# Performance work log

Measured on AMD Instinct MI355X. Metric: run time of the kernel, lower is better.

Reference implementation:

```python
import jax, jax.numpy as jnp
import numpy as np

N = 4096        # atoms
F = 128         # node feature channels (MACE hidden irreps scalar channels)
K = 8           # radial basis size
NELEM = 10      # chemical elements
RMAX = 5.0      # cutoff (Angstrom), model.r_max
BOX = 34.5      # box side -> ~0.1 atoms/A^3, ~50 neighbors within RMAX


def setup_inputs() -> dict:
    key = jax.random.key(0)
    ks = jax.random.split(key, 7)
    positions = jax.random.uniform(ks[0], (N, 3), jnp.float32) * BOX
    z = jax.random.randint(ks[1], (N,), 0, NELEM)
    embed = jax.random.normal(ks[2], (NELEM, F), jnp.float32) * 0.1
    W1 = jax.random.normal(ks[3], (K, F, F), jnp.float32) / np.sqrt(K * F)
    W2 = jax.random.normal(ks[4], (K, F, F), jnp.float32) / np.sqrt(K * F)
    Wr1 = jax.random.normal(ks[5], (F, F), jnp.float32) / np.sqrt(F)
    Wr2 = jax.random.normal(ks[6], (F, 1), jnp.float32) / np.sqrt(F)
    return dict(positions=positions, z=z, embed=embed, W1=W1, W2=W2, Wr1=Wr1, Wr2=Wr2)


def _energy(positions, embed, W1, W2, Wr1, Wr2, z):
    # node embedding from atomic species (node_attrs one-hot @ embedding)
    h = embed[z]                                            # [N,F]
    # --- neighborlist: radius graph with self-edge masking (pbc = False) ---
    sq = jnp.sum(positions * positions, axis=-1)            # [N]
    d2 = sq[:, None] + sq[None, :] - 2.0 * (positions @ positions.T)  # [N,N]
    eye = jnp.eye(positions.shape[0], dtype=bool)
    d2_safe = jnp.where(eye | (d2 <= 0), 1.0, d2)           # avoid sqrt(0) grad
    d = jnp.sqrt(d2_safe)                                   # [N,N]
    mask = (d < RMAX) & (~eye) & (d2 > 0)                   # keep_edge = ~true_self_edge
    # smooth cutoff envelope
    env = jnp.where(mask, 0.5 * (jnp.cos(jnp.pi * d / RMAX) + 1.0), 0.0)  # [N,N]
    # Gaussian radial basis
    mus = jnp.linspace(0.0, RMAX, K, dtype=jnp.float32)     # [K]
    gamma = jnp.float32((K / RMAX) ** 2)
    rbf = jnp.exp(-gamma * (d[..., None] - mus) ** 2) * env[..., None]    # [N,N,K]
    # --- two message-passing layers (radial-weighted neighbor aggregation) ---
    for W in (W1, W2):
        A = jnp.einsum('ijk,jf->ikf', rbf, h)               # [N,K,F] gather-scatter agg
        h = jax.nn.silu(jnp.einsum('ikf,kfg->ig', A, W) + h)  # [N,F]
    # --- per-atom energy readout, summed over graph ---
    e_atom = (jax.nn.silu(h @ Wr1) @ Wr2)[:, 0]             # [N]
    return jnp.sum(e_atom)


def reference(positions, z, embed, W1, W2, Wr1, Wr2):
    energy, dE_dpos = jax.value_and_grad(_energy)(positions, embed, W1, W2, Wr1, Wr2, z)
    forces = -dE_dpos                                       # [N,3]
    return energy, forces
```

## Files before the change

kernel.cpp:

```cpp
#include <hip/hip_runtime.h>
#include <math.h>

#define N_ATOMS 4096
#define F 128
#define K 8
#define KF 1024
#define KFF 131072
#define FF 16384
#define NF 524288
#define NF4 131072
#define NKF 4194304
#define MAXNB 128
#define RMAX 5.0f
#define GAMMA 2.56f
#define MU_STEP 0.714285714285714f
#define PI_F 3.14159265358979323846f
#define POR (PI_F / RMAX)

typedef __bf16 bf16x8_t __attribute__((ext_vector_type(8)));
typedef float f32x4_t __attribute__((ext_vector_type(4)));
typedef unsigned short u16x8_t __attribute__((ext_vector_type(8)));
typedef unsigned short u16x4_t __attribute__((ext_vector_type(4)));

__device__ __forceinline__ float sigm(float x){ return 1.0f/(1.0f + expf(-x)); }
__device__ __forceinline__ unsigned short f2bf(float x){
  unsigned int u = __float_as_uint(x);
  u += 0x7fff + ((u >> 16) & 1);
  return (unsigned short)(u >> 16);
}

__global__ __launch_bounds__(256) void k_nb(const float* __restrict__ pos,
        int* __restrict__ nb_idx, float* __restrict__ nb_d, int* __restrict__ nb_cnt){
  int t = threadIdx.x;
  int w = t >> 6, lane = t & 63;
  int i = blockIdx.x*4 + w;
  __shared__ float spx[256], spy[256], spz[256], ssq[256];
  float pix = pos[3*i], piy = pos[3*i+1], piz = pos[3*i+2];
  float sqi = pix*pix + piy*piy + piz*piz;
  int count = 0;
  for (int jb = 0; jb < N_ATOMS; jb += 256){
    __syncthreads();
    float px = pos[3*(jb+t)], py = pos[3*(jb+t)+1], pz = pos[3*(jb+t)+2];
    spx[t] = px; spy[t] = py; spz[t] = pz;
    ssq[t] = px*px + py*py + pz*pz;
    __syncthreads();
    #pragma unroll
    for (int c = 0; c < 4; c++){
      int jj = c*64 + lane;
      int j = jb + jj;
      float dot = pix*spx[jj] + piy*spy[jj] + piz*spz[jj];
      float d2 = sqi + ssq[jj] - 2.0f*dot;
      float d = sqrtf(d2);
      bool pred = (j != i) && (d2 > 0.0f) && (d < RMAX);
      unsigned long long m = __ballot(pred);
      int off = __popcll(m & ((1ull << lane) - 1ull));
      if (pred){
        int p = count + off;
        if (p < MAXNB){ nb_idx[i*MAXNB + p] = j; nb_d[i*MAXNB + p] = d; }
      }
      count += __popcll(m);
    }
  }
  if (lane == 0) nb_cnt[i] = count > MAXNB ? MAXNB : count;
}

__global__ __launch_bounds__(64) void k_rbf(const float* __restrict__ nb_d,
        const int* __restrict__ nb_cnt, float* __restrict__ rbf,
        float* __restrict__ drbf){
  int a = blockIdx.x;
  int cnt = nb_cnt[a];
  for (int n = threadIdx.x; n < cnt; n += 64){
    float d = nb_d[a*MAXNB + n];
    float ph = POR*d;
    float cph, sph;
    __sincosf(ph, &sph, &cph);
    float env = 0.5f*(cph + 1.0f);
    float denv = -0.5f*POR*sph;
    float rr[8], dd[8];
    #pragma unroll
    for (int k = 0; k < 8; k++){
      float dm = d - MU_STEP*(float)k;
      float G = expf(-GAMMA*dm*dm);
      rr[k] = G*env;
      dd[k] = G*(-2.0f*GAMMA*dm*env + denv);
    }
    float4* rb = (float4*)(rbf + ((size_t)a*MAXNB + n)*8);
    rb[0] = {rr[0],rr[1],rr[2],rr[3]};
    rb[1] = {rr[4],rr[5],rr[6],rr[7]};
    float4* db = (float4*)(drbf + ((size_t)a*MAXNB + n)*8);
    db[0] = {dd[0],dd[1],dd[2],dd[3]};
    db[1] = {dd[4],dd[5],dd[6],dd[7]};
  }
}

__global__ __launch_bounds__(256) void k_wprep(const float* __restrict__ W1,
        const float* __restrict__ W2, const float* __restrict__ Wr1,
        const int* __restrict__ z, const float* __restrict__ embed,
        unsigned short* __restrict__ WF1, unsigned short* __restrict__ WF2,
        unsigned short* __restrict__ WDF2, unsigned short* __restrict__ WTF1,
        unsigned short* __restrict__ WTF2, unsigned short* __restrict__ Wr1F,
        unsigned short* __restrict__ Wr1TF,
        float* __restrict__ h0, unsigned short* __restrict__ h0bf){
  if (blockIdx.x >= 64){
    int idx = (blockIdx.x - 64)*256 + threadIdx.x;
    int i = idx >> 7, f = idx & 127;
    float v = embed[z[i]*F + f];
    h0[idx] = v;
    h0bf[idx] = f2bf(v);
    return;
  }
  int idx = blockIdx.x*256 + threadIdx.x;
  int l = idx & 63;
  int hi = idx >> 6;
  {
    int kc = hi >> 3, nt = hi & 7;
    int kfb = kc*32 + ((l>>4)&3)*8;
    int g = nt*16 + (l&15);
    u16x8_t v1, v2, vd;
    #pragma unroll
    for (int j = 0; j < 8; j++){
      int kf = kfb + j;
      v1[j] = f2bf(W1[kf*128 + g]);
      v2[j] = f2bf(W2[kf*128 + g]);
      vd[j] = f2bf(W2[(kf>>7)*FF + g*F + (kf&127)]);
    }
    *(u16x8_t*)(WF1 + idx*8) = v1;
    *(u16x8_t*)(WF2 + idx*8) = v2;
    *(u16x8_t*)(WDF2 + idx*8) = vd;
  }
  {
    int kc = hi >> 6, nt = hi & 63;
    int gb = kc*32 + ((l>>4)&3)*8;
    int kf = nt*16 + (l&15);
    u16x8_t t1, t2;
    #pragma unroll
    for (int j = 0; j < 8; j++){
      int g = gb + j;
      t1[j] = f2bf(W1[kf*128 + g]);
      t2[j] = f2bf(W2[kf*128 + g]);
    }
    *(u16x8_t*)(WTF1 + idx*8) = t1;
    *(u16x8_t*)(WTF2 + idx*8) = t2;
  }
  {
    int m = idx >> 9;
    int ll = (idx >> 3) & 63;
    int j = idx & 7;
    int kc = m >> 3, nt = m & 7;
    int kf = kc*32 + ((ll>>4)&3)*8 + j;
    int g = nt*16 + (ll&15);
    Wr1F[idx]  = f2bf(Wr1[kf*128 + g]);
    Wr1TF[idx] = f2bf(Wr1[g*128 + kf]);
  }
}

__global__ __launch_bounds__(256) void k_agg(const float* __restrict__ h_in,
        const int* __restrict__ nb_idx, const float* __restrict__ rbf,
        const int* __restrict__ nb_cnt, unsigned short* __restrict__ Af){
  int a = blockIdx.x;
  int t = threadIdx.x;
  int grp = t >> 6, lane = t & 63;
  __shared__ int s_j[MAXNB];
  __shared__ float s_acc[4][8][128];
  int cnt = nb_cnt[a];
  for (int idx = t; idx < cnt; idx += 256) s_j[idx] = nb_idx[a*MAXNB + idx];
  __syncthreads();
  float2 acc[8];
  #pragma unroll
  for (int k = 0; k < 8; k++) acc[k] = {0.f, 0.f};
  const float4* rb = (const float4*)(rbf + (size_t)a*MAXNB*8);
  for (int n = grp; n < cnt; n += 4){
    float2 hv = *(const float2*)&h_in[(size_t)s_j[n]*F + lane*2];
    float4 r0 = rb[n*2], r1 = rb[n*2+1];
    acc[0].x += r0.x*hv.x; acc[0].y += r0.x*hv.y;
    acc[1].x += r0.y*hv.x; acc[1].y += r0.y*hv.y;
    acc[2].x += r0.z*hv.x; acc[2].y += r0.z*hv.y;
    acc[3].x += r0.w*hv.x; acc[3].y += r0.w*hv.y;
    acc[4].x += r1.x*hv.x; acc[4].y += r1.x*hv.y;
    acc[5].x += r1.y*hv.x; acc[5].y += r1.y*hv.y;
    acc[6].x += r1.z*hv.x; acc[6].y += r1.z*hv.y;
    acc[7].x += r1.w*hv.x; acc[7].y += r1.w*hv.y;
  }
  #pragma unroll
  for (int k = 0; k < 8; k++)
    *(float2*)&s_acc[grp][k][lane*2] = acc[k];
  __syncthreads();
  int k = t >> 5, q = t & 31;
  int f0 = q*4;
  float v[4];
  #pragma unroll
  for (int i = 0; i < 4; i++){
    int f = f0 + i;
    v[i] = s_acc[0][k][f] + s_acc[1][k][f] + s_acc[2][k][f] + s_acc[3][k][f];
  }
  int lf = (a & 15) | (((f0 >> 3) & 3) << 4);
  int kc = k*4 + (f0 >> 5);
  size_t flat = (size_t)(a >> 4)*16384 + ((size_t)kc*64 + lf)*8 + (f0 & 7);
  u16x4_t o;
  o[0] = f2bf(v[0]); o[1] = f2bf(v[1]); o[2] = f2bf(v[2]); o[3] = f2bf(v[3]);
  *(u16x4_t*)(Af + flat) = o;
}

__global__ __launch_bounds__(256) void k_mgemm_fwd(const unsigned short* __restrict__ Af,
        const unsigned short* __restrict__ Bf, const float* __restrict__ addv,
        const float* __restrict__ msrc, float* __restrict__ out_m,
        float* __restrict__ out_h, unsigned short* __restrict__ out_hbf,
        unsigned short* __restrict__ out_frag, int mode){
  int t = threadIdx.x;
  int l = t & 63, w = t >> 6;
  int rtile = blockIdx.x;
  int nt = blockIdx.y*4 + w;
  f32x4_t accA = (f32x4_t){0.f,0.f,0.f,0.f};
  f32x4_t accB = (f32x4_t){0.f,0.f,0.f,0.f};
  const unsigned short* Ab = Af + (size_t)rtile*16384 + l*8;
  const unsigned short* Bb = Bf + l*8;
  #pragma unroll
  for (int kc = 0; kc < 32; kc += 2){
    bf16x8_t a0 = *(const bf16x8_t*)(Ab + kc*512);
    bf16x8_t b0 = *(const bf16x8_t*)(Bb + (kc*8 + nt)*512);
    bf16x8_t a1 = *(const bf16x8_t*)(Ab + (kc+1)*512);
    bf16x8_t b1 = *(const bf16x8_t*)(Bb + ((kc+1)*8 + nt)*512);
    accA = __builtin_amdgcn_mfma_f32_16x16x32_bf16(a0, b0, accA, 0, 0, 0);
    accB = __builtin_amdgcn_mfma_f32_16x16x32_bf16(a1, b1, accB, 0, 0, 0);
  }
  f32x4_t acc = accA + accB;
  int row0 = rtile*16 + (l >> 4)*4;
  int col = nt*16 + (l & 15);
  if (mode == 0){
    #pragma unroll
    for (int r = 0; r < 4; r++){
      int i = row0 + r;
      float m = acc[r] + addv[(size_t)i*F + col];
      out_m[(size_t)i*F + col] = m;
      float h = m*sigm(m);
      out_h[(size_t)i*F + col] = h;
      out_hbf[(size_t)i*F + col] = f2bf(h);
    }
  } else {
    int kc2 = col >> 5;
    int lfr0 = (((col >> 3) & 3) << 4);
    int jj = col & 7;
    #pragma unroll
    for (int r = 0; r < 4; r++){
      int i = row0 + r;
      float mm = msrc[(size_t)i*F + col];
      float sg = sigm(mm);
      float gv = (acc[r] + addv[(size_t)i*F + col])*(sg*(1.f + mm*(1.f - sg)));
      int lfr = (i & 15) | lfr0;
      size_t flat = (((size_t)(i>>4)*4 + kc2)*64 + lfr)*8 + jj;
      out_frag[flat] = f2bf(gv);
    }
  }
}

__global__ __launch_bounds__(256) void k_mgemm_bwd(const unsigned short* __restrict__ Gf,
        const unsigned short* __restrict__ Bf, unsigned short* __restrict__ dAbf){
  int t = threadIdx.x;
  int l = t & 63, w = t >> 6;
  int rtile = blockIdx.x*4 + w;
  int nt0 = blockIdx.y*8;
  f32x4_t acc[8];
  #pragma unroll
  for (int i = 0; i < 8; i++) acc[i] = (f32x4_t){0.f,0.f,0.f,0.f};
  const unsigned short* Ab = Gf + (size_t)rtile*2048 + l*8;
  const unsigned short* Bb = Bf + l*8;
  #pragma unroll
  for (int kc = 0; kc < 4; kc++){
    bf16x8_t a = *(const bf16x8_t*)(Ab + kc*512);
    #pragma unroll
    for (int nt = 0; nt < 8; nt++){
      bf16x8_t b = *(const bf16x8_t*)(Bb + (kc*64 + nt0 + nt)*512);
      acc[nt] = __builtin_amdgcn_mfma_f32_16x16x32_bf16(a, b, acc[nt], 0, 0, 0);
    }
  }
  int row0 = rtile*16 + (l >> 4)*4;
  int col = l & 15;
  #pragma unroll
  for (int nt = 0; nt < 8; nt++){
    #pragma unroll
    for (int r = 0; r < 4; r++)
      dAbf[(size_t)(row0+r)*1024 + (nt0+nt)*16 + col] = f2bf(acc[nt][r]);
  }
}

__global__ __launch_bounds__(64) void k_readout(const unsigned short* __restrict__ h2bf,
        const float* __restrict__ m2, const unsigned short* __restrict__ Wr1F,
        const unsigned short* __restrict__ Wr1TF, const float* __restrict__ Wr2,
        float* __restrict__ e_at, float* __restrict__ g2,
        unsigned short* __restrict__ g2frag){
  int a0 = blockIdx.x*16;
  int l = threadIdx.x;
  int rl = l & 15, sel = (l >> 4) & 3;
  __shared__ unsigned short sdu[16][136];
  f32x4_t acc[8];
  #pragma unroll
  for (int nt = 0; nt < 8; nt++) acc[nt] = (f32x4_t){0.f,0.f,0.f,0.f};
  #pragma unroll
  for (int kc = 0; kc < 4; kc++){
    bf16x8_t af = *(const bf16x8_t*)(h2bf + (size_t)(a0+rl)*F + kc*32 + sel*8);
    #pragma unroll
    for (int nt = 0; nt < 8; nt++){
      bf16x8_t bf = *(const bf16x8_t*)(Wr1F + ((kc*8+nt)*64 + l)*8);
      acc[nt] = __builtin_amdgcn_mfma_f32_16x16x32_bf16(af, bf, acc[nt], 0, 0, 0);
    }
  }
  float epart[4] = {0.f,0.f,0.f,0.f};
  #pragma unroll
  for (int nt = 0; nt < 8; nt++){
    float w2 = Wr2[nt*16 + rl];
    #pragma unroll
    for (int r = 0; r < 4; r++){
      float u = acc[nt][r];
      float sg = sigm(u);
      epart[r] += u*sg*w2;
      sdu[(l>>4)*4 + r][nt*16 + rl] = f2bf(w2*(sg*(1.f + u*(1.f - sg))));
    }
  }
  #pragma unroll
  for (int o = 1; o < 16; o <<= 1){
    #pragma unroll
    for (int r = 0; r < 4; r++) epart[r] += __shfl_xor(epart[r], o);
  }
  if (rl == 0){
    #pragma unroll
    for (int r = 0; r < 4; r++) e_at[a0 + (l>>4)*4 + r] = epart[r];
  }
  __syncthreads();
  f32x4_t acc2[8];
  #pragma unroll
  for (int nt = 0; nt < 8; nt++) acc2[nt] = (f32x4_t){0.f,0.f,0.f,0.f};
  #pragma unroll
  for (int kc = 0; kc < 4; kc++){
    bf16x8_t af = *(const bf16x8_t*)&sdu[rl][kc*32 + sel*8];
    #pragma unroll
    for (int nt = 0; nt < 8; nt++){
      bf16x8_t bf = *(const bf16x8_t*)(Wr1TF + ((kc*8+nt)*64 + l)*8);
      acc2[nt] = __builtin_amdgcn_mfma_f32_16x16x32_bf16(af, bf, acc2[nt], 0, 0, 0);
    }
  }
  #pragma unroll
  for (int nt = 0; nt < 8; nt++){
    int g = nt*16 + rl;
    int kc2 = g >> 5;
    int lfr0 = (((g >> 3) & 3) << 4);
    int jj = g & 7;
    #pragma unroll
    for (int r = 0; r < 4; r++){
      int a = a0 + (l>>4)*4 + r;
      float mm = m2[(size_t)a*F + g];
      float sg = sigm(mm);
      float gv = acc2[nt][r]*(sg*(1.f + mm*(1.f - sg)));
      g2[(size_t)a*F + g] = gv;
      int lfr = (a & 15) | lfr0;
      g2frag[(((size_t)(a>>4)*4 + kc2)*64 + lfr)*8 + jj] = f2bf(gv);
    }
  }
}

__global__ __launch_bounds__(256) void k_edge(const unsigned short* __restrict__ dA2bf,
        const unsigned short* __restrict__ dA1bf, const unsigned short* __restrict__ h1bf,
        const unsigned short* __restrict__ h0bf, const float* __restrict__ drbf,
        const int* __restrict__ nb_idx, const int* __restrict__ nb_cnt,
        float* __restrict__ edge_s){
  int a = blockIdx.x;
  int t = threadIdx.x;
  int w = t >> 6, l = t & 63;
  __shared__ int s_j[MAXNB];
  int cnt = nb_cnt[a];
  for (int idx = t; idx < cnt; idx += 256) s_j[idx] = nb_idx[a*MAXNB + idx];
  int r = l & 15;
  int sel = (l >> 4) & 3;
  u16x8_t a2u[4], a1u[4];
  #pragma unroll
  for (int kc = 0; kc < 4; kc++){
    u16x8_t v2 = {0,0,0,0,0,0,0,0};
    u16x8_t v1 = {0,0,0,0,0,0,0,0};
    if (r < 8){
      v2 = *(const u16x8_t*)(dA2bf + (size_t)a*KF + r*F + kc*32 + sel*8);
      v1 = *(const u16x8_t*)(dA1bf + (size_t)a*KF + r*F + kc*32 + sel*8);
    }
    a2u[kc] = v2; a1u[kc] = v1;
  }
  __syncthreads();
  for (int n0 = w*16; n0 < cnt; n0 += 64){
    int nl = n0 + r;
    int nls = nl < cnt ? nl : cnt - 1;
    int j = s_j[nls];
    const unsigned short* h1p = h1bf + (size_t)j*F + sel*8;
    const unsigned short* h0p = h0bf + (size_t)j*F + sel*8;
    f32x4_t acc = (f32x4_t){0.f,0.f,0.f,0.f};
    #pragma unroll
    for (int kc = 0; kc < 4; kc++){
      bf16x8_t b = *(const bf16x8_t*)(h1p + kc*32);
      acc = __builtin_amdgcn_mfma_f32_16x16x32_bf16(*(const bf16x8_t*)&a2u[kc], b, acc, 0, 0, 0);
    }
    #pragma unroll
    for (int kc = 0; kc < 4; kc++){
      bf16x8_t b = *(const bf16x8_t*)(h0p + kc*32);
      acc = __builtin_amdgcn_mfma_f32_16x16x32_bf16(*(const bf16x8_t*)&a1u[kc], b, acc, 0, 0, 0);
    }
    int krow = (l >> 4) * 4;
    float part = 0.f;
    if (krow < 8){
      float4 dr = *(const float4*)(drbf + ((size_t)a*MAXNB + nls)*8 + krow);
      part = acc[0]*dr.x + acc[1]*dr.y + acc[2]*dr.z + acc[3]*dr.w;
    }
    part += __shfl_xor(part, 16);
    if (l < 16 && nl < cnt) edge_s[a*MAXNB + nl] = part;
  }
}

__global__ __launch_bounds__(64) void k_force(const float* __restrict__ pos,
        const int* __restrict__ nb_idx, const float* __restrict__ nb_d,
        const int* __restrict__ nb_cnt, const float* __restrict__ edge_s,
        const float* __restrict__ e_at, float* __restrict__ out){
  int a = blockIdx.x;
  int lane = threadIdx.x;
  if (a == N_ATOMS){
    float s = 0.f;
    for (int i = lane; i < N_ATOMS; i += 64) s += e_at[i];
    #pragma unroll
    for (int o = 1; o < 64; o <<= 1) s += __shfl_xor(s, o);
    if (lane == 0) out[0] = s;
    return;
  }
  float pax = pos[3*a], pay = pos[3*a+1], paz = pos[3*a+2];
  int cnt = nb_cnt[a];
  float fx = 0.f, fy = 0.f, fz = 0.f;
  for (int n = lane; n < cnt; n += 64){
    int j = nb_idx[a*MAXNB + n];
    float d = nb_d[a*MAXNB + n];
    float s = edge_s[a*MAXNB + n];
    int cj = nb_cnt[j];
    int lo = 0, hi = cj - 1, p = -1;
    while (lo <= hi){
      int mid = (lo + hi) >> 1;
      int v = nb_idx[j*MAXNB + mid];
      if (v == a){ p = mid; break; }
      if (v < a) lo = mid + 1; else hi = mid - 1;
    }
    float sj = (p >= 0) ? edge_s[j*MAXNB + p] : 0.0f;
    float coef = (s + sj)/d;
    float dx = pax - pos[3*j], dy = pay - pos[3*j+1], dz = paz - pos[3*j+2];
    fx -= coef*dx; fy -= coef*dy; fz -= coef*dz;
  }
  #pragma unroll
  for (int o = 1; o < 64; o <<= 1){
    fx += __shfl_xor(fx, o); fy += __shfl_xor(fy, o); fz += __shfl_xor(fz, o);
  }
  if (lane == 0){
    out[1 + 3*a + 0] = fx;
    out[1 + 3*a + 1] = fy;
    out[1 + 3*a + 2] = fz;
  }
}

extern "C" void kernel_launch(void* const* d_in, const int* in_sizes, int n_in,
                              void* d_out, int out_size, void* d_ws, size_t ws_size,
                              hipStream_t stream){
  const float* pos   = (const float*)d_in[0];
  const int*   z     = (const int*)  d_in[1];
  const float* embed = (const float*)d_in[2];
  const float* W1    = (const float*)d_in[3];
  const float* W2    = (const float*)d_in[4];
  const float* Wr1   = (const float*)d_in[5];
  const float* Wr2   = (const float*)d_in[6];
  float* out = (float*)d_out;

  float* ws = (float*)d_ws;
  float* h0   = ws;
  float* h1   = h0 + NF;
  float* h2   = h1 + NF;
  float* m1   = h2 + NF;
  float* m2   = m1 + NF;
  float* g2b  = m2 + NF;
  float* Bbuf = g2b + NF;
  float* Cbuf = Bbuf + NKF;
  unsigned short* dA2bf = (unsigned short*)Bbuf;
  unsigned short* dA1bf = (unsigned short*)Cbuf;
  unsigned short* Afrag = (unsigned short*)(Cbuf + NKF);
  unsigned short* Gfrag = Afrag + NKF;
  unsigned short* h0bf = Gfrag + NF;
  unsigned short* h1bf = h0bf + NF;
  unsigned short* h2bf = h1bf + NF;
  unsigned short* WF1  = h2bf + NF;
  unsigned short* WF2  = WF1 + KFF;
  unsigned short* WDF2 = WF2 + KFF;
  unsigned short* WTF1 = WDF2 + KFF;
  unsigned short* WTF2 = WTF1 + KFF;
  unsigned short* Wr1F  = WTF2 + KFF;
  unsigned short* Wr1TF = Wr1F + FF;
  float* e_at = (float*)(Wr1TF + FF);
  float* nb_d = e_at + N_ATOMS;
  float* edge_s = nb_d + N_ATOMS*MAXNB;
  float* rbf  = edge_s + N_ATOMS*MAXNB;
  float* drbf = rbf + N_ATOMS*MAXNB*8;
  int* nb_idx = (int*)(drbf + N_ATOMS*MAXNB*8);
  int* nb_cnt = nb_idx + N_ATOMS*MAXNB;

  k_nb<<<N_ATOMS/4, 256, 0, stream>>>(pos, nb_idx, nb_d, nb_cnt);
  k_rbf<<<N_ATOMS, 64, 0, stream>>>(nb_d, nb_cnt, rbf, drbf);
  k_wprep<<<64 + NF/256, 256, 0, stream>>>(W1, W2, Wr1, z, embed,
        WF1, WF2, WDF2, WTF1, WTF2, Wr1F, Wr1TF, h0, h0bf);

  k_agg<<<N_ATOMS, 256, 0, stream>>>(h0, nb_idx, rbf, nb_cnt, Afrag);
  k_mgemm_fwd<<<dim3(256, 2), 256, 0, stream>>>(Afrag, WF1, h0, h0, m1, h1, h1bf, Gfrag, 0);
  k_agg<<<N_ATOMS, 256, 0, stream>>>(h1, nb_idx, rbf, nb_cnt, Afrag);
  k_mgemm_fwd<<<dim3(256, 2), 256, 0, stream>>>(Afrag, WF2, h1, h1, m2, h2, h2bf, Gfrag, 0);

  k_readout<<<N_ATOMS/16, 64, 0, stream>>>(h2bf, m2, Wr1F, Wr1TF, Wr2, e_at, g2b, Gfrag);

  k_mgemm_bwd<<<dim3(64, 8), 256, 0, stream>>>(Gfrag, WTF2, dA2bf);
  k_agg<<<N_ATOMS, 256, 0, stream>>>(g2b, nb_idx, rbf, nb_cnt, Afrag);
  k_mgemm_fwd<<<dim3(256, 2), 256, 0, stream>>>(Afrag, WDF2, g2b, m1, m1, m1, h2bf, Gfrag, 1);
  k_mgemm_bwd<<<dim3(64, 8), 256, 0, stream>>>(Gfrag, WTF1, dA1bf);
  k_edge<<<N_ATOMS, 256, 0, stream>>>(dA2bf, dA1bf, h1bf, h0bf, drbf, nb_idx, nb_cnt, edge_s);
  k_force<<<N_ATOMS + 1, 64, 0, stream>>>(pos, nb_idx, nb_d, nb_cnt, edge_s, e_at, out);
}
```

Before: 207.0 us.

## Merge prep kernels and co-launch backward GEMM with aggregation

Folds neighbor search, RBF evaluation and weight/embedding prep into one launch, with the RBF computed by the same wave right after it builds its neighbor list. Also merges the independent layer-2 backward GEMM and the gradient aggregation into one grid split by block index. This cuts kernel launches and the idle gaps between them, and lets independent work fill the GPU together. In exchange the fused kernels take the larger shared-memory and register footprint of their branches, and prep blocks become imbalanced, with neighbor-search blocks doing much more work than weight-prep blocks.

Result: faster. 187.9 us (-9.2%).

```diff
diff --git a/kernel.cpp b/kernel.cpp
--- a/kernel.cpp
+++ b/kernel.cpp
@@ -8,7 +8,6 @@
 #define KFF 131072
 #define FF 16384
 #define NF 524288
-#define NF4 131072
 #define NKF 4194304
 #define MAXNB 128
 #define RMAX 5.0f
@@ -29,136 +28,11 @@
   return (unsigned short)(u >> 16);
 }
 
-__global__ __launch_bounds__(256) void k_nb(const float* __restrict__ pos,
-        int* __restrict__ nb_idx, float* __restrict__ nb_d, int* __restrict__ nb_cnt){
-  int t = threadIdx.x;
-  int w = t >> 6, lane = t & 63;
-  int i = blockIdx.x*4 + w;
-  __shared__ float spx[256], spy[256], spz[256], ssq[256];
-  float pix = pos[3*i], piy = pos[3*i+1], piz = pos[3*i+2];
-  float sqi = pix*pix + piy*piy + piz*piz;
-  int count = 0;
-  for (int jb = 0; jb < N_ATOMS; jb += 256){
-    __syncthreads();
-    float px = pos[3*(jb+t)], py = pos[3*(jb+t)+1], pz = pos[3*(jb+t)+2];
-    spx[t] = px; spy[t] = py; spz[t] = pz;
-    ssq[t] = px*px + py*py + pz*pz;
-    __syncthreads();
-    #pragma unroll
-    for (int c = 0; c < 4; c++){
-      int jj = c*64 + lane;
-      int j = jb + jj;
-      float dot = pix*spx[jj] + piy*spy[jj] + piz*spz[jj];
-      float d2 = sqi + ssq[jj] - 2.0f*dot;
-      float d = sqrtf(d2);
-      bool pred = (j != i) && (d2 > 0.0f) && (d < RMAX);
-      unsigned long long m = __ballot(pred);
-      int off = __popcll(m & ((1ull << lane) - 1ull));
-      if (pred){
-        int p = count + off;
-        if (p < MAXNB){ nb_idx[i*MAXNB + p] = j; nb_d[i*MAXNB + p] = d; }
-      }
-      count += __popcll(m);
-    }
-  }
-  if (lane == 0) nb_cnt[i] = count > MAXNB ? MAXNB : count;
-}
-
-__global__ __launch_bounds__(64) void k_rbf(const float* __restrict__ nb_d,
-        const int* __restrict__ nb_cnt, float* __restrict__ rbf,
-        float* __restrict__ drbf){
-  int a = blockIdx.x;
-  int cnt = nb_cnt[a];
-  for (int n = threadIdx.x; n < cnt; n += 64){
-    float d = nb_d[a*MAXNB + n];
-    float ph = POR*d;
-    float cph, sph;
-    __sincosf(ph, &sph, &cph);
-    float env = 0.5f*(cph + 1.0f);
-    float denv = -0.5f*POR*sph;
-    float rr[8], dd[8];
-    #pragma unroll
-    for (int k = 0; k < 8; k++){
-      float dm = d - MU_STEP*(float)k;
-      float G = expf(-GAMMA*dm*dm);
-      rr[k] = G*env;
-      dd[k] = G*(-2.0f*GAMMA*dm*env + denv);
-    }
-    float4* rb = (float4*)(rbf + ((size_t)a*MAXNB + n)*8);
-    rb[0] = {rr[0],rr[1],rr[2],rr[3]};
-    rb[1] = {rr[4],rr[5],rr[6],rr[7]};
-    float4* db = (float4*)(drbf + ((size_t)a*MAXNB + n)*8);
-    db[0] = {dd[0],dd[1],dd[2],dd[3]};
-    db[1] = {dd[4],dd[5],dd[6],dd[7]};
-  }
-}
-
-__global__ __launch_bounds__(256) void k_wprep(const float* __restrict__ W1,
-        const float* __restrict__ W2, const float* __restrict__ Wr1,
-        const int* __restrict__ z, const float* __restrict__ embed,
-        unsigned short* __restrict__ WF1, unsigned short* __restrict__ WF2,
-        unsigned short* __restrict__ WDF2, unsigned short* __restrict__ WTF1,
-        unsigned short* __restrict__ WTF2, unsigned short* __restrict__ Wr1F,
-        unsigned short* __restrict__ Wr1TF,
-        float* __restrict__ h0, unsigned short* __restrict__ h0bf){
-  if (blockIdx.x >= 64){
-    int idx = (blockIdx.x - 64)*256 + threadIdx.x;
-    int i = idx >> 7, f = idx & 127;
-    float v = embed[z[i]*F + f];
-    h0[idx] = v;
-    h0bf[idx] = f2bf(v);
-    return;
-  }
-  int idx = blockIdx.x*256 + threadIdx.x;
-  int l = idx & 63;
-  int hi = idx >> 6;
-  {
-    int kc = hi >> 3, nt = hi & 7;
-    int kfb = kc*32 + ((l>>4)&3)*8;
-    int g = nt*16 + (l&15);
-    u16x8_t v1, v2, vd;
-    #pragma unroll
-    for (int j = 0; j < 8; j++){
-      int kf = kfb + j;
-      v1[j] = f2bf(W1[kf*128 + g]);
-      v2[j] = f2bf(W2[kf*128 + g]);
-      vd[j] = f2bf(W2[(kf>>7)*FF + g*F + (kf&127)]);
-    }
-    *(u16x8_t*)(WF1 + idx*8) = v1;
-    *(u16x8_t*)(WF2 + idx*8) = v2;
-    *(u16x8_t*)(WDF2 + idx*8) = vd;
-  }
-  {
-    int kc = hi >> 6, nt = hi & 63;
-    int gb = kc*32 + ((l>>4)&3)*8;
-    int kf = nt*16 + (l&15);
-    u16x8_t t1, t2;
-    #pragma unroll
-    for (int j = 0; j < 8; j++){
-      int g = gb + j;
-      t1[j] = f2bf(W1[kf*128 + g]);
-      t2[j] = f2bf(W2[kf*128 + g]);
-    }
-    *(u16x8_t*)(WTF1 + idx*8) = t1;
-    *(u16x8_t*)(WTF2 + idx*8) = t2;
-  }
-  {
-    int m = idx >> 9;
-    int ll = (idx >> 3) & 63;
-    int j = idx & 7;
-    int kc = m >> 3, nt = m & 7;
-    int kf = kc*32 + ((ll>>4)&3)*8 + j;
-    int g = nt*16 + (ll&15);
-    Wr1F[idx]  = f2bf(Wr1[kf*128 + g]);
-    Wr1TF[idx] = f2bf(Wr1[g*128 + kf]);
-  }
-}
-
-__global__ __launch_bounds__(256) void k_agg(const float* __restrict__ h_in,
-        const int* __restrict__ nb_idx, const float* __restrict__ rbf,
-        const int* __restrict__ nb_cnt, unsigned short* __restrict__ Af){
-  int a = blockIdx.x;
-  int t = threadIdx.x;
+
+__device__ __forceinline__ void agg_body(int a, int t,
+        const float* __restrict__ h_in, const int* __restrict__ nb_idx,
+        const float* __restrict__ rbf, const int* __restrict__ nb_cnt,
+        unsigned short* __restrict__ Af){
   int grp = t >> 6, lane = t & 63;
   __shared__ int s_j[MAXNB];
   __shared__ float s_acc[4][8][128];
@@ -201,6 +75,182 @@
   *(u16x4_t*)(Af + flat) = o;
 }
 
+__device__ __forceinline__ void mgemm_bwd_body(int bx, int t,
+        const unsigned short* __restrict__ Gf, const unsigned short* __restrict__ Bf,
+        unsigned short* __restrict__ dAbf){
+  int l = t & 63, w = t >> 6;
+  int rtile = (bx & 63)*4 + w;
+  int nt0 = (bx >> 6)*8;
+  f32x4_t acc[8];
+  #pragma unroll
+  for (int i = 0; i < 8; i++) acc[i] = (f32x4_t){0.f,0.f,0.f,0.f};
+  const unsigned short* Ab = Gf + (size_t)rtile*2048 + l*8;
+  const unsigned short* Bb = Bf + l*8;
+  #pragma unroll
+  for (int kc = 0; kc < 4; kc++){
+    bf16x8_t a = *(const bf16x8_t*)(Ab + kc*512);
+    #pragma unroll
+    for (int nt = 0; nt < 8; nt++){
+      bf16x8_t b = *(const bf16x8_t*)(Bb + (kc*64 + nt0 + nt)*512);
+      acc[nt] = __builtin_amdgcn_mfma_f32_16x16x32_bf16(a, b, acc[nt], 0, 0, 0);
+    }
+  }
+  int row0 = rtile*16 + (l >> 4)*4;
+  int col = l & 15;
+  #pragma unroll
+  for (int nt = 0; nt < 8; nt++){
+    #pragma unroll
+    for (int r = 0; r < 4; r++)
+      dAbf[(size_t)(row0+r)*1024 + (nt0+nt)*16 + col] = f2bf(acc[nt][r]);
+  }
+}
+
+
+__global__ __launch_bounds__(256) void k_prep(const float* __restrict__ pos,
+        const int* __restrict__ z, const float* __restrict__ embed,
+        const float* __restrict__ W1, const float* __restrict__ W2,
+        const float* __restrict__ Wr1,
+        int* __restrict__ nb_idx, float* __restrict__ nb_d, int* __restrict__ nb_cnt,
+        float* __restrict__ rbf, float* __restrict__ drbf,
+        unsigned short* __restrict__ WF1, unsigned short* __restrict__ WF2,
+        unsigned short* __restrict__ WDF2, unsigned short* __restrict__ WTF1,
+        unsigned short* __restrict__ WTF2, unsigned short* __restrict__ Wr1F,
+        unsigned short* __restrict__ Wr1TF,
+        float* __restrict__ h0, unsigned short* __restrict__ h0bf){
+  int t = threadIdx.x;
+  if (blockIdx.x < 1024){
+    int w = t >> 6, lane = t & 63;
+    int i = blockIdx.x*4 + w;
+    __shared__ float spx[256], spy[256], spz[256], ssq[256];
+    float pix = pos[3*i], piy = pos[3*i+1], piz = pos[3*i+2];
+    float sqi = pix*pix + piy*piy + piz*piz;
+    int count = 0;
+    for (int jb = 0; jb < N_ATOMS; jb += 256){
+      __syncthreads();
+      float px = pos[3*(jb+t)], py = pos[3*(jb+t)+1], pz = pos[3*(jb+t)+2];
+      spx[t] = px; spy[t] = py; spz[t] = pz;
+      ssq[t] = px*px + py*py + pz*pz;
+      __syncthreads();
+      #pragma unroll
+      for (int c = 0; c < 4; c++){
+        int jj = c*64 + lane;
+        int j = jb + jj;
+        float dot = pix*spx[jj] + piy*spy[jj] + piz*spz[jj];
+        float d2 = sqi + ssq[jj] - 2.0f*dot;
+        float d = sqrtf(d2);
+        bool pred = (j != i) && (d2 > 0.0f) && (d < RMAX);
+        unsigned long long m = __ballot(pred);
+        int off = __popcll(m & ((1ull << lane) - 1ull));
+        if (pred){
+          int p = count + off;
+          if (p < MAXNB){ nb_idx[i*MAXNB + p] = j; nb_d[i*MAXNB + p] = d; }
+        }
+        count += __popcll(m);
+      }
+    }
+    int cc = count > MAXNB ? MAXNB : count;
+    if (lane == 0) nb_cnt[i] = cc;
+    __syncthreads();
+    for (int n = lane; n < cc; n += 64){
+      float d = nb_d[i*MAXNB + n];
+      float ph = POR*d;
+      float cph, sph;
+      __sincosf(ph, &sph, &cph);
+      float env = 0.5f*(cph + 1.0f);
+      float denv = -0.5f*POR*sph;
+      float rr[8], dd[8];
+      #pragma unroll
+      for (int k = 0; k < 8; k++){
+        float dm = d - MU_STEP*(float)k;
+        float G = expf(-GAMMA*dm*dm);
+        rr[k] = G*env;
+        dd[k] = G*(-2.0f*GAMMA*dm*env + denv);
+      }
+      float4* rb = (float4*)(rbf + ((size_t)i*MAXNB + n)*8);
+      rb[0] = {rr[0],rr[1],rr[2],rr[3]};
+      rb[1] = {rr[4],rr[5],rr[6],rr[7]};
+      float4* db = (float4*)(drbf + ((size_t)i*MAXNB + n)*8);
+      db[0] = {dd[0],dd[1],dd[2],dd[3]};
+      db[1] = {dd[4],dd[5],dd[6],dd[7]};
+    }
+    return;
+  }
+  if (blockIdx.x >= 1088){
+    int idx = (blockIdx.x - 1088)*256 + t;
+    int i = idx >> 7, f = idx & 127;
+    float v = embed[z[i]*F + f];
+    h0[idx] = v;
+    h0bf[idx] = f2bf(v);
+    return;
+  }
+  int idx = (blockIdx.x - 1024)*256 + t;
+  int l = idx & 63;
+  int hi = idx >> 6;
+  {
+    int kc = hi >> 3, nt = hi & 7;
+    int kfb = kc*32 + ((l>>4)&3)*8;
+    int g = nt*16 + (l&15);
+    u16x8_t v1, v2, vd;
+    #pragma unroll
+    for (int j = 0; j < 8; j++){
+      int kf = kfb + j;
+      v1[j] = f2bf(W1[kf*128 + g]);
+      v2[j] = f2bf(W2[kf*128 + g]);
+      vd[j] = f2bf(W2[(kf>>7)*FF + g*F + (kf&127)]);
+    }
+    *(u16x8_t*)(WF1 + idx*8) = v1;
+    *(u16x8_t*)(WF2 + idx*8) = v2;
+    *(u16x8_t*)(WDF2 + idx*8) = vd;
+  }
+  {
+    int kc = hi >> 6, nt = hi & 63;
+    int gb = kc*32 + ((l>>4)&3)*8;
+    int kf = nt*16 + (l&15);
+    u16x8_t t1, t2;
+    #pragma unroll
+    for (int j = 0; j < 8; j++){
+      int g = gb + j;
+      t1[j] = f2bf(W1[kf*128 + g]);
+      t2[j] = f2bf(W2[kf*128 + g]);
+    }
+    *(u16x8_t*)(WTF1 + idx*8) = t1;
+    *(u16x8_t*)(WTF2 + idx*8) = t2;
+  }
+  {
+    int m = idx >> 9;
+    int ll = (idx >> 3) & 63;
+    int j = idx & 7;
+    int kc = m >> 3, nt = m & 7;
+    int kf = kc*32 + ((ll>>4)&3)*8 + j;
+    int g = nt*16 + (ll&15);
+    Wr1F[idx]  = f2bf(Wr1[kf*128 + g]);
+    Wr1TF[idx] = f2bf(Wr1[g*128 + kf]);
+  }
+}
+
+__global__ __launch_bounds__(256) void k_agg(const float* __restrict__ h_in,
+        const int* __restrict__ nb_idx, const float* __restrict__ rbf,
+        const int* __restrict__ nb_cnt, unsigned short* __restrict__ Af){
+  agg_body(blockIdx.x, threadIdx.x, h_in, nb_idx, rbf, nb_cnt, Af);
+}
+
+__global__ __launch_bounds__(256) void k_bwdmix(const unsigned short* __restrict__ Gf,
+        const unsigned short* __restrict__ Bf, unsigned short* __restrict__ dAbf,
+        const float* __restrict__ g2b, const int* __restrict__ nb_idx,
+        const float* __restrict__ rbf, const int* __restrict__ nb_cnt,
+        unsigned short* __restrict__ Af){
+  if (blockIdx.x < 512){
+    mgemm_bwd_body(blockIdx.x, threadIdx.x, Gf, Bf, dAbf);
+    return;
+  }
+  agg_body(blockIdx.x - 512, threadIdx.x, g2b, nb_idx, rbf, nb_cnt, Af);
+}
+
+__global__ __launch_bounds__(256) void k_mgemm_bwd(const unsigned short* __restrict__ Gf,
+        const unsigned short* __restrict__ Bf, unsigned short* __restrict__ dAbf){
+  mgemm_bwd_body(blockIdx.x, threadIdx.x, Gf, Bf, dAbf);
+}
+
 __global__ __launch_bounds__(256) void k_mgemm_fwd(const unsigned short* __restrict__ Af,
         const unsigned short* __restrict__ Bf, const float* __restrict__ addv,
         const float* __restrict__ msrc, float* __restrict__ out_m,
@@ -253,36 +303,6 @@
   }
 }
 
-__global__ __launch_bounds__(256) void k_mgemm_bwd(const unsigned short* __restrict__ Gf,
-        const unsigned short* __restrict__ Bf, unsigned short* __restrict__ dAbf){
-  int t = threadIdx.x;
-  int l = t & 63, w = t >> 6;
-  int rtile = blockIdx.x*4 + w;
-  int nt0 = blockIdx.y*8;
-  f32x4_t acc[8];
-  #pragma unroll
-  for (int i = 0; i < 8; i++) acc[i] = (f32x4_t){0.f,0.f,0.f,0.f};
-  const unsigned short* Ab = Gf + (size_t)rtile*2048 + l*8;
-  const unsigned short* Bb = Bf + l*8;
-  #pragma unroll
-  for (int kc = 0; kc < 4; kc++){
-    bf16x8_t a = *(const bf16x8_t*)(Ab + kc*512);
-    #pragma unroll
-    for (int nt = 0; nt < 8; nt++){
-      bf16x8_t b = *(const bf16x8_t*)(Bb + (kc*64 + nt0 + nt)*512);
-      acc[nt] = __builtin_amdgcn_mfma_f32_16x16x32_bf16(a, b, acc[nt], 0, 0, 0);
-    }
-  }
-  int row0 = rtile*16 + (l >> 4)*4;
-  int col = l & 15;
-  #pragma unroll
-  for (int nt = 0; nt < 8; nt++){
-    #pragma unroll
-    for (int r = 0; r < 4; r++)
-      dAbf[(size_t)(row0+r)*1024 + (nt0+nt)*16 + col] = f2bf(acc[nt][r]);
-  }
-}
-
 __global__ __launch_bounds__(64) void k_readout(const unsigned short* __restrict__ h2bf,
         const float* __restrict__ m2, const unsigned short* __restrict__ Wr1F,
         const unsigned short* __restrict__ Wr1TF, const float* __restrict__ Wr2,
@@ -290,14 +310,14 @@
         unsigned short* __restrict__ g2frag){
   int a0 = blockIdx.x*16;
   int l = threadIdx.x;
-  int rl = l & 15, sel = (l >> 4) & 3;
+  int rl = l & 15;
   __shared__ unsigned short sdu[16][136];
   f32x4_t acc[8];
   #pragma unroll
   for (int nt = 0; nt < 8; nt++) acc[nt] = (f32x4_t){0.f,0.f,0.f,0.f};
   #pragma unroll
   for (int kc = 0; kc < 4; kc++){
-    bf16x8_t af = *(const bf16x8_t*)(h2bf + (size_t)(a0+rl)*F + kc*32 + sel*8);
+    bf16x8_t af = *(const bf16x8_t*)(h2bf + (size_t)(a0+rl)*F + kc*32 + ((l>>4)&3)*8);
     #pragma unroll
     for (int nt = 0; nt < 8; nt++){
       bf16x8_t bf = *(const bf16x8_t*)(Wr1F + ((kc*8+nt)*64 + l)*8);
@@ -331,7 +351,7 @@
   for (int nt = 0; nt < 8; nt++) acc2[nt] = (f32x4_t){0.f,0.f,0.f,0.f};
   #pragma unroll
   for (int kc = 0; kc < 4; kc++){
-    bf16x8_t af = *(const bf16x8_t*)&sdu[rl][kc*32 + sel*8];
+    bf16x8_t af = *(const bf16x8_t*)&sdu[rl][kc*32 + ((l>>4)&3)*8];
     #pragma unroll
     for (int nt = 0; nt < 8; nt++){
       bf16x8_t bf = *(const bf16x8_t*)(Wr1TF + ((kc*8+nt)*64 + l)*8);
@@ -498,9 +518,8 @@
   int* nb_idx = (int*)(drbf + N_ATOMS*MAXNB*8);
   int* nb_cnt = nb_idx + N_ATOMS*MAXNB;
 
-  k_nb<<<N_ATOMS/4, 256, 0, stream>>>(pos, nb_idx, nb_d, nb_cnt);
-  k_rbf<<<N_ATOMS, 64, 0, stream>>>(nb_d, nb_cnt, rbf, drbf);
-  k_wprep<<<64 + NF/256, 256, 0, stream>>>(W1, W2, Wr1, z, embed,
+  k_prep<<<1024 + 64 + NF/256, 256, 0, stream>>>(pos, z, embed, W1, W2, Wr1,
+        nb_idx, nb_d, nb_cnt, rbf, drbf,
         WF1, WF2, WDF2, WTF1, WTF2, Wr1F, Wr1TF, h0, h0bf);
 
   k_agg<<<N_ATOMS, 256, 0, stream>>>(h0, nb_idx, rbf, nb_cnt, Afrag);
@@ -510,10 +529,10 @@
 
   k_readout<<<N_ATOMS/16, 64, 0, stream>>>(h2bf, m2, Wr1F, Wr1TF, Wr2, e_at, g2b, Gfrag);
 
-  k_mgemm_bwd<<<dim3(64, 8), 256, 0, stream>>>(Gfrag, WTF2, dA2bf);
-  k_agg<<<N_ATOMS, 256, 0, stream>>>(g2b, nb_idx, rbf, nb_cnt, Afrag);
+  k_bwdmix<<<512 + N_ATOMS, 256, 0, stream>>>(Gfrag, WTF2, dA2bf,
+        g2b, nb_idx, rbf, nb_cnt, Afrag);
   k_mgemm_fwd<<<dim3(256, 2), 256, 0, stream>>>(Afrag, WDF2, g2b, m1, m1, m1, h2bf, Gfrag, 1);
-  k_mgemm_bwd<<<dim3(64, 8), 256, 0, stream>>>(Gfrag, WTF1, dA1bf);
+  k_mgemm_bwd<<<512, 256, 0, stream>>>(Gfrag, WTF1, dA1bf);
   k_edge<<<N_ATOMS, 256, 0, stream>>>(dA2bf, dA1bf, h1bf, h0bf, drbf, nb_idx, nb_cnt, edge_s);
   k_force<<<N_ATOMS + 1, 64, 0, stream>>>(pos, nb_idx, nb_d, nb_cnt, edge_s, e_at, out);
 }
```
